# Kernel optimization log

Hardware: AMD Instinct MI355X
Metric: run time of the kernel (lower is better)

## Reference

```python
import jax, jax.numpy as jnp
import numpy as np
import math

D_MODEL = 1024
N_HEADS = 16
D_KV = 64
INNER = N_HEADS * D_KV
NUM_BUCKETS = 32
MAX_DISTANCE = 128


def _relative_position_bucket(relative_position, bidirectional=True,
                              num_buckets=NUM_BUCKETS, max_distance=MAX_DISTANCE):
    # faithful port of T5Attention._relative_position_bucket
    relative_buckets = jnp.zeros_like(relative_position)
    if bidirectional:
        num_buckets //= 2
        relative_buckets = relative_buckets + (relative_position > 0).astype(jnp.int32) * num_buckets
        relative_position = jnp.abs(relative_position)
    else:
        relative_position = -jnp.minimum(relative_position, jnp.zeros_like(relative_position))
    max_exact = num_buckets // 2
    is_small = relative_position < max_exact
    rp_large = max_exact + (
        jnp.log(relative_position.astype(jnp.float32) / max_exact)
        / math.log(max_distance / max_exact) * (num_buckets - max_exact)
    ).astype(jnp.int32)
    rp_large = jnp.minimum(rp_large, num_buckets - 1)
    return relative_buckets + jnp.where(is_small, relative_position, rp_large)


def compute_bias(rel_bias_table, q_len, k_len):
    # [q_len, k_len] relative positions -> bucket ids -> [1, H, q_len, k_len] bias
    context = jnp.arange(q_len, dtype=jnp.int32)[:, None]
    memory = jnp.arange(k_len, dtype=jnp.int32)[None, :]
    buckets = _relative_position_bucket(memory - context, bidirectional=True)
    values = rel_bias_table[buckets]            # [q, k, H]
    return jnp.transpose(values, (2, 0, 1))[None]  # [1, H, q, k]


def setup_inputs() -> dict:
    key = jax.random.key(0)
    ks = jax.random.split(key, 6)
    B, S = 2, 2048
    scale = 0.02
    return {
        "hidden_states": jax.random.normal(ks[0], (B, S, D_MODEL), jnp.float32),
        # weights stored as [in, out] (torch Linear applies x @ W.T with W [out,in])
        "w_q": jax.random.normal(ks[1], (D_MODEL, INNER), jnp.float32) * scale,
        "w_k": jax.random.normal(ks[2], (D_MODEL, INNER), jnp.float32) * scale,
        "w_v": jax.random.normal(ks[3], (D_MODEL, INNER), jnp.float32) * scale,
        "w_o": jax.random.normal(ks[4], (INNER, D_MODEL), jnp.float32) * scale,
        "rel_bias_table": jax.random.normal(ks[5], (NUM_BUCKETS, N_HEADS), jnp.float32) * scale,
    }


def reference(hidden_states, w_q, w_k, w_v, w_o, rel_bias_table):
    B, S, _ = hidden_states.shape

    def shape(x):  # [B, S, inner] -> [B, H, S, d_kv]
        return jnp.transpose(x.reshape(B, S, N_HEADS, D_KV), (0, 2, 1, 3))

    q = shape(hidden_states @ w_q)  # note: T5 applies no 1/sqrt(d) scaling
    k = shape(hidden_states @ w_k)
    v = shape(hidden_states @ w_v)

    scores = jnp.einsum("bhqd,bhkd->bhqk", q, k)
    position_bias = compute_bias(rel_bias_table, S, S)
    scores = scores + position_bias
    attn = jax.nn.softmax(scores.astype(jnp.float32), axis=-1).astype(scores.dtype)
    ctx = jnp.einsum("bhqk,bhkd->bhqd", attn, v)
    ctx = jnp.transpose(ctx, (0, 2, 1, 3)).reshape(B, S, INNER)
    return ctx @ w_o
```

## Files before the change

kernel.cpp:

```cpp
#include <hip/hip_runtime.h>
#include <math.h>

#define S_LEN 2048
#define DM 1024

typedef __attribute__((ext_vector_type(8))) __bf16 bf16x8;
typedef __attribute__((ext_vector_type(4))) float floatx4;

typedef __attribute__((address_space(1))) const unsigned int g_u32;
typedef __attribute__((address_space(3))) unsigned int l_u32;

__device__ __forceinline__ unsigned short f2bf(float f) {
  union { float f; unsigned int u; } v; v.f = f;
  return (unsigned short)((v.u + 0x7fffu + ((v.u >> 16) & 1u)) >> 16);
}
__device__ __forceinline__ float bf2f(unsigned short u) {
  union { unsigned int u; float f; } v; v.u = ((unsigned int)u) << 16;
  return v.f;
}
__device__ __forceinline__ bf16x8 ld_frag(const unsigned short* p) {
  union { uint4 u; bf16x8 v; } t;
  t.u = *(const uint4*)p;
  return t.v;
}

__global__ void detect_k(const unsigned short* __restrict__ x, int* __restrict__ flag) {
  __shared__ int cnt;
  if (threadIdx.x == 0) cnt = 0;
  __syncthreads();
  int local = 0;
  for (int i = threadIdx.x; i < 4096; i += 256) {
    unsigned short u = x[i];
    int e = (u >> 7) & 0xFF;
    if (e > 140) local++;
  }
  atomicAdd(&cnt, local);
  __syncthreads();
  if (threadIdx.x == 0) *flag = (cnt > 64) ? 1 : 0;
}

__global__ void conv_bias(const void* __restrict__ src, unsigned short* __restrict__ dst,
                          const void* __restrict__ table, float* __restrict__ outb,
                          const int* __restrict__ flag) {
  const int bid = blockIdx.x, tid = threadIdx.x;
  if (bid < 2048) {
    int i = bid * 256 + tid;
    if (*flag) {
      const float4* s = (const float4*)src;
      float4 a = s[2 * i], b = s[2 * i + 1];
      union { uint4 u4; unsigned short s[8]; } o;
      o.s[0] = f2bf(a.x); o.s[1] = f2bf(a.y); o.s[2] = f2bf(a.z); o.s[3] = f2bf(a.w);
      o.s[4] = f2bf(b.x); o.s[5] = f2bf(b.y); o.s[6] = f2bf(b.z); o.s[7] = f2bf(b.w);
      ((uint4*)dst)[i] = o.u4;
    } else {
      ((uint4*)dst)[i] = ((const uint4*)src)[i];
    }
  } else {
    int idx = (bid - 2048) * 256 + tid;
    if (idx >= 16 * 384) return;
    int h = idx / 384;
    int j = idx - h * 384;
    int delta = j - 192;
    int bucket = (delta > 0) ? 16 : 0;
    int ad = (delta < 0) ? -delta : delta;
    int smallv;
    if (ad < 8) smallv = ad;
    else {
      int l = (int)(log((double)ad * 0.125) * (8.0 / log(16.0)));
      smallv = 8 + l;
      if (smallv > 15) smallv = 15;
    }
    bucket += smallv;
    float v;
    if (*flag) v = ((const float*)table)[bucket * 16 + h];
    else       v = bf2f(((const unsigned short*)table)[bucket * 16 + h]);
    outb[idx] = v * 1.44269504f - 24.f;
  }
}

__global__ void transpose_w(const void* __restrict__ s0, const void* __restrict__ s1,
                            const void* __restrict__ s2, const void* __restrict__ s3,
                            unsigned short* __restrict__ Wcat, unsigned short* __restrict__ Wto,
                            const int* __restrict__ flag) {
  __shared__ float tile[32][33];
  const int z = blockIdx.z;
  const void* src = (z == 0) ? s0 : (z == 1) ? s1 : (z == 2) ? s2 : s3;
  unsigned short* dst = (z < 3) ? (Wcat + (size_t)z * 1048576) : Wto;
  const int isf = *flag;
  int x = blockIdx.x * 32 + threadIdx.x;
  int y0 = blockIdx.y * 32;
  for (int i = threadIdx.y; i < 32; i += 8) {
    float v;
    if (isf) v = ((const float*)src)[(size_t)(y0 + i) * DM + x];
    else     v = bf2f(((const unsigned short*)src)[(size_t)(y0 + i) * DM + x]);
    tile[i][threadIdx.x] = v;
  }
  __syncthreads();
  int xo = y0 + threadIdx.x;
  for (int i = threadIdx.y; i < 32; i += 8)
    dst[(size_t)(blockIdx.x * 32 + i) * DM + xo] = f2bf(tile[threadIdx.x][i]);
}

__global__ __launch_bounds__(256) void gemm_bt(
    const unsigned short* __restrict__ A, const unsigned short* __restrict__ Bt,
    void* __restrict__ C)
{
  __shared__ __align__(16) unsigned short smem[128 * 136];
  unsigned short* As = smem;
  unsigned short* Bs = smem + 8192;
  const int tid = threadIdx.x;
  const int lane = tid & 63, wave = tid >> 6;
  const int l16 = lane & 15, quad = lane >> 4;
  const int wm = (wave >> 1) << 6, wn = (wave & 1) << 6;
  const int m0 = blockIdx.y << 7, n0 = blockIdx.x << 7;
  const int lrow = lane >> 3, lcol = (lane & 7) << 3;

  floatx4 acc[4][4] = {};

  for (int k0 = 0; k0 < 1024; k0 += 64) {
    __syncthreads();
#pragma unroll
    for (int i = 0; i < 4; ++i) {
      int r0 = wave * 32 + i * 8;
      __builtin_amdgcn_global_load_lds(
          (g_u32*)(const void*)(A + (size_t)(m0 + r0 + lrow) * 1024 + k0 + lcol),
          (l_u32*)(void*)&As[r0 * 64], 16, 0, 0);
      __builtin_amdgcn_global_load_lds(
          (g_u32*)(const void*)(Bt + (size_t)(n0 + r0 + lrow) * 1024 + k0 + lcol),
          (l_u32*)(void*)&Bs[r0 * 64], 16, 0, 0);
    }
    __syncthreads();
#pragma unroll
    for (int ks = 0; ks < 2; ++ks) {
      bf16x8 a[4], b[4];
#pragma unroll
      for (int mi = 0; mi < 4; ++mi)
        a[mi] = *(const bf16x8*)&As[(wm + mi * 16 + l16) * 64 + ks * 32 + quad * 8];
#pragma unroll
      for (int ni = 0; ni < 4; ++ni)
        b[ni] = *(const bf16x8*)&Bs[(wn + ni * 16 + l16) * 64 + ks * 32 + quad * 8];
#pragma unroll
      for (int mi = 0; mi < 4; ++mi)
#pragma unroll
        for (int ni = 0; ni < 4; ++ni)
          acc[mi][ni] = __builtin_amdgcn_mfma_f32_16x16x32_bf16(a[mi], b[ni], acc[mi][ni], 0, 0, 0);
    }
  }

  unsigned short* Cs = (unsigned short*)C;
  const int mat = n0 >> 10;
  if (mat < 2) {
#pragma unroll
    for (int mi = 0; mi < 4; ++mi)
#pragma unroll
      for (int ni = 0; ni < 4; ++ni)
#pragma unroll
        for (int i = 0; i < 4; ++i) {
          int m = m0 + wm + mi * 16 + quad * 4 + i;
          int n = (n0 & 1023) + wn + ni * 16 + l16;
          int b = m >> 11, s = m & 2047, h = n >> 6, d = n & 63;
          Cs[(size_t)mat * 4194304 + (((size_t)(b * 16 + h)) * 2048 + s) * 64 + d] =
              f2bf(acc[mi][ni][i]);
        }
  } else {
    __syncthreads();
#pragma unroll
    for (int mi = 0; mi < 4; ++mi)
#pragma unroll
      for (int ni = 0; ni < 4; ++ni) {
        union { unsigned short s[4]; uint2 u; } w;
#pragma unroll
        for (int i = 0; i < 4; ++i) w.s[i] = f2bf(acc[mi][ni][i]);
        *(uint2*)&smem[(wn + ni * 16 + l16) * 136 + wm + mi * 16 + quad * 4] = w.u;
      }
    __syncthreads();
    const int bb = m0 >> 11, s0 = m0 & 2047, nb = n0 & 1023;
#pragma unroll
    for (int it = 0; it < 8; ++it) {
      int r = it * 16 + (tid >> 4);
      int c = (tid & 15) * 8;
      uint4 rv = *(const uint4*)&smem[r * 136 + c];
      *(uint4*)&Cs[(size_t)2 * 4194304 + (size_t)(bb * 1024 + nb + r) * 2048 + s0 + c] = rv;
    }
  }
}

__global__ __launch_bounds__(256) void gemm_out(
    const unsigned short* __restrict__ A, const unsigned short* __restrict__ Bt,
    void* __restrict__ C, const int* __restrict__ flag)
{
  __shared__ __align__(16) unsigned short As[128 * 64];
  __shared__ __align__(16) unsigned short Bs[64 * 64];
  const int tid = threadIdx.x;
  const int lane = tid & 63, wave = tid >> 6;
  const int l16 = lane & 15, quad = lane >> 4;
  const int wm = (wave >> 1) << 6, wn = (wave & 1) << 5;
  const int m0 = blockIdx.y << 7, n0 = blockIdx.x << 6;
  const int lrow = lane >> 3, lcol = (lane & 7) << 3;

  floatx4 acc[4][2] = {};

  for (int k0 = 0; k0 < 1024; k0 += 64) {
    __syncthreads();
#pragma unroll
    for (int i = 0; i < 4; ++i) {
      int r0 = wave * 32 + i * 8;
      __builtin_amdgcn_global_load_lds(
          (g_u32*)(const void*)(A + (size_t)(m0 + r0 + lrow) * 1024 + k0 + lcol),
          (l_u32*)(void*)&As[r0 * 64], 16, 0, 0);
    }
#pragma unroll
    for (int i = 0; i < 2; ++i) {
      int r0 = wave * 16 + i * 8;
      __builtin_amdgcn_global_load_lds(
          (g_u32*)(const void*)(Bt + (size_t)(n0 + r0 + lrow) * 1024 + k0 + lcol),
          (l_u32*)(void*)&Bs[r0 * 64], 16, 0, 0);
    }
    __syncthreads();
#pragma unroll
    for (int ks = 0; ks < 2; ++ks) {
      bf16x8 a[4], b[2];
#pragma unroll
      for (int mi = 0; mi < 4; ++mi)
        a[mi] = *(const bf16x8*)&As[(wm + mi * 16 + l16) * 64 + ks * 32 + quad * 8];
#pragma unroll
      for (int ni = 0; ni < 2; ++ni)
        b[ni] = *(const bf16x8*)&Bs[(wn + ni * 16 + l16) * 64 + ks * 32 + quad * 8];
#pragma unroll
      for (int mi = 0; mi < 4; ++mi)
#pragma unroll
        for (int ni = 0; ni < 2; ++ni)
          acc[mi][ni] = __builtin_amdgcn_mfma_f32_16x16x32_bf16(a[mi], b[ni], acc[mi][ni], 0, 0, 0);
    }
  }

  const int isf = *flag;
#pragma unroll
  for (int mi = 0; mi < 4; ++mi)
#pragma unroll
    for (int ni = 0; ni < 2; ++ni)
#pragma unroll
      for (int i = 0; i < 4; ++i) {
        int m = m0 + wm + mi * 16 + quad * 4 + i;
        int n = n0 + wn + ni * 16 + l16;
        size_t idx = (size_t)m * 1024 + n;
        float v = acc[mi][ni][i];
        if (isf) ((float*)C)[idx] = v;
        else     ((unsigned short*)C)[idx] = f2bf(v);
      }
}

#define STAGE_KV(kv0, buf)                                                    \
  {                                                                           \
    int rr = tid >> 3;                                                        \
    int sw = ((tid & 7) ^ (rr & 7)) << 3;                                     \
    __builtin_amdgcn_global_load_lds(                                         \
        (g_u32*)(const void*)(Kp + (size_t)((kv0) + rr) * 64 + sw),           \
        (l_u32*)(void*)&Ks[buf][wave * 512], 16, 0, 0);                       \
    __builtin_amdgcn_global_load_lds(                                         \
        (g_u32*)(const void*)(Vp + (size_t)rr * S_LEN + (kv0) + sw),          \
        (l_u32*)(void*)&Vs[buf][wave * 512], 16, 0, 0);                       \
  }

__global__ __launch_bounds__(512, 4) void attn_k(
    const unsigned short* __restrict__ Q, const unsigned short* __restrict__ K,
    const unsigned short* __restrict__ Vt, const float* __restrict__ bias,
    unsigned short* __restrict__ ctx)
{
  __shared__ __align__(16) unsigned short Ks[2][4096];
  __shared__ __align__(16) unsigned short Vs[2][4096];
  __shared__ __align__(16) unsigned short Ps[8][16][72];
  __shared__ float Bls[384];
  const int tid = threadIdx.x;
  const int lane = tid & 63, wave = tid >> 6;
  const int l16 = lane & 15, quad = lane >> 4;
  const int bh = blockIdx.y;
  const int b = bh >> 4, h = bh & 15;
  const int q0 = blockIdx.x << 7;
  const int wq = wave << 4;

  const unsigned short* Qp = Q + (size_t)bh * S_LEN * 64;
  const unsigned short* Kp = K + (size_t)bh * S_LEN * 64;
  const unsigned short* Vp = Vt + (size_t)bh * 64 * S_LEN;
  const float* biasg = bias + h * 384;

  STAGE_KV(0, 0);
  if (tid < 384) Bls[tid] = biasg[tid];

  bf16x8 qf[2];
#pragma unroll
  for (int ks = 0; ks < 2; ++ks)
    qf[ks] = ld_frag(Qp + (size_t)(q0 + wq + l16) * 64 + ks * 32 + quad * 8);

  float l_run[4] = {};
  floatx4 oacc[4] = {};

  const int qwb = q0 + wq;
  const int rbase = 192 + l16 - (quad << 2) - qwb;

  __syncthreads();
  const float Bneg = Bls[0], Bpos = Bls[383];

  for (int kv0 = 0; kv0 < S_LEN; kv0 += 64) {
    const int cur = (kv0 >> 6) & 1;
    if (kv0 + 64 < S_LEN) STAGE_KV(kv0 + 64, cur ^ 1);

    floatx4 sac[4] = {};
#pragma unroll
    for (int ks = 0; ks < 2; ++ks) {
      bf16x8 kf[4];
#pragma unroll
      for (int ni = 0; ni < 4; ++ni)
        kf[ni] = *(const bf16x8*)&Ks[cur][(ni * 16 + l16) * 64 +
                                          ((((ks << 2) + quad) ^ (l16 & 7)) << 3)];
#pragma unroll
      for (int ni = 0; ni < 4; ++ni)
        sac[ni] = __builtin_amdgcn_mfma_f32_16x16x32_bf16(qf[ks], kf[ni], sac[ni], 0, 0, 0);
    }

    {
      const int dmin = kv0 - (qwb + 15);
      const int dmax = kv0 + 63 - qwb;
      if (dmin >= 96 || dmax <= -96) {
        const float bc = (dmin >= 96) ? Bpos : Bneg;
#pragma unroll
        for (int i = 0; i < 4; ++i) {
          float sum = 0.f;
#pragma unroll
          for (int ni = 0; ni < 4; ++ni) {
            float e = __builtin_amdgcn_exp2f(fmaf(sac[ni][i], 1.44269504f, bc));
            sac[ni][i] = e; sum += e;
          }
          l_run[i] += sum;
        }
      } else {
#pragma unroll
        for (int i = 0; i < 4; ++i) {
          const int bbase = kv0 + rbase - i;
          float sum = 0.f;
#pragma unroll
          for (int ni = 0; ni < 4; ++ni) {
            float e = __builtin_amdgcn_exp2f(
                fmaf(sac[ni][i], 1.44269504f, Bls[bbase + ni * 16]));
            sac[ni][i] = e; sum += e;
          }
          l_run[i] += sum;
        }
      }
    }

#pragma unroll
    for (int ni = 0; ni < 4; ++ni)
#pragma unroll
      for (int i = 0; i < 4; ++i)
        Ps[wave][quad * 4 + i][ni * 16 + l16] = f2bf(sac[ni][i]);

#pragma unroll
    for (int ks2 = 0; ks2 < 2; ++ks2) {
      bf16x8 af, vf[4];
      af = *(const bf16x8*)&Ps[wave][l16][ks2 * 32 + quad * 8];
#pragma unroll
      for (int ni = 0; ni < 4; ++ni)
        vf[ni] = *(const bf16x8*)&Vs[cur][(ni * 16 + l16) * 64 +
                                          ((((ks2 << 2) + quad) ^ (l16 & 7)) << 3)];
#pragma unroll
      for (int ni = 0; ni < 4; ++ni)
        oacc[ni] = __builtin_amdgcn_mfma_f32_16x16x32_bf16(af, vf[ni], oacc[ni], 0, 0, 0);
    }

    __syncthreads();
  }

  float linv[4];
#pragma unroll
  for (int i = 0; i < 4; ++i) {
    float ls = l_run[i];
    ls += __shfl_xor(ls, 1);
    ls += __shfl_xor(ls, 2);
    ls += __shfl_xor(ls, 4);
    ls += __shfl_xor(ls, 8);
    linv[i] = 1.f / ls;
  }

#pragma unroll
  for (int ni = 0; ni < 4; ++ni)
#pragma unroll
    for (int i = 0; i < 4; ++i) {
      float v = oacc[ni][i] * linv[i];
      int srow = q0 + wq + quad * 4 + i;
      ctx[((size_t)(b * 2048 + srow)) * 1024 + h * 64 + ni * 16 + l16] = f2bf(v);
    }
}

extern "C" void kernel_launch(void* const* d_in, const int* in_sizes, int n_in,
                              void* d_out, int out_size, void* d_ws, size_t ws_size,
                              hipStream_t stream) {
  char* ws = (char*)d_ws;
  unsigned short* Xbf  = (unsigned short*)(ws);
  unsigned short* Wcat = (unsigned short*)(ws + 8388608);
  unsigned short* Wto  = (unsigned short*)(ws + 14680064);
  unsigned short* Qb   = (unsigned short*)(ws + 16777216);
  unsigned short* ctx  = (unsigned short*)(ws + 41943040);
  float*          bias = (float*)(ws + 50331648);
  int*            flag = (int*)(ws + 50593792);

  unsigned short* Kb  = Qb + 4194304;
  unsigned short* Vtb = Qb + 8388608;

  detect_k<<<1, 256, 0, stream>>>((const unsigned short*)d_in[0], flag);
  conv_bias<<<2072, 256, 0, stream>>>(d_in[0], Xbf, d_in[5], bias, flag);
  transpose_w<<<dim3(32, 32, 4), dim3(32, 8), 0, stream>>>(
      d_in[1], d_in[2], d_in[3], d_in[4], Wcat, Wto, flag);

  gemm_bt<<<dim3(24, 32), 256, 0, stream>>>(Xbf, Wcat, Qb);

  attn_k<<<dim3(16, 32), 512, 0, stream>>>(Qb, Kb, Vtb, bias, ctx);

  gemm_out<<<dim3(16, 32), 256, 0, stream>>>(ctx, Wto, d_out, flag);
}
```

Before: 222.4 us.

## Fuse prep kernels, compute softmax row sums via MFMA, use native bf16 convert

Merges the input conversion, bias table and weight transpose kernels into one prep launch, cutting launch overhead. Replaces the detect kernel with a host-side check on input size plus a memset when the size matches. In attention, the per-row exp sums are now taken by an extra MFMA against a ones vector instead of scalar adds and shuffles, which frees VALU work at the cost of one more MFMA per k-step. Float-to-bf16 conversion now uses the native cast.

```diff
diff --git a/kernel.cpp b/kernel.cpp
--- a/kernel.cpp
+++ b/kernel.cpp
@@ -11,8 +11,9 @@
 typedef __attribute__((address_space(3))) unsigned int l_u32;
 
 __device__ __forceinline__ unsigned short f2bf(float f) {
-  union { float f; unsigned int u; } v; v.f = f;
-  return (unsigned short)((v.u + 0x7fffu + ((v.u >> 16) & 1u)) >> 16);
+  union { __bf16 h; unsigned short u; } v;
+  v.h = (__bf16)f;
+  return v.u;
 }
 __device__ __forceinline__ float bf2f(unsigned short u) {
   union { unsigned int u; float f; } v; v.u = ((unsigned int)u) << 16;
@@ -39,23 +40,27 @@
   if (threadIdx.x == 0) *flag = (cnt > 64) ? 1 : 0;
 }
 
-__global__ void conv_bias(const void* __restrict__ src, unsigned short* __restrict__ dst,
-                          const void* __restrict__ table, float* __restrict__ outb,
-                          const int* __restrict__ flag) {
+__global__ void prep_k(const void* __restrict__ x, unsigned short* __restrict__ dst,
+                       const void* __restrict__ tbl, float* __restrict__ outb,
+                       const void* __restrict__ w0, const void* __restrict__ w1,
+                       const void* __restrict__ w2, const void* __restrict__ w3,
+                       unsigned short* __restrict__ Wcat, unsigned short* __restrict__ Wto,
+                       const int* __restrict__ flag) {
+  __shared__ float tile[32][33];
   const int bid = blockIdx.x, tid = threadIdx.x;
   if (bid < 2048) {
     int i = bid * 256 + tid;
     if (*flag) {
-      const float4* s = (const float4*)src;
+      const float4* s = (const float4*)x;
       float4 a = s[2 * i], b = s[2 * i + 1];
       union { uint4 u4; unsigned short s[8]; } o;
       o.s[0] = f2bf(a.x); o.s[1] = f2bf(a.y); o.s[2] = f2bf(a.z); o.s[3] = f2bf(a.w);
       o.s[4] = f2bf(b.x); o.s[5] = f2bf(b.y); o.s[6] = f2bf(b.z); o.s[7] = f2bf(b.w);
       ((uint4*)dst)[i] = o.u4;
     } else {
-      ((uint4*)dst)[i] = ((const uint4*)src)[i];
-    }
-  } else {
+      ((uint4*)dst)[i] = ((const uint4*)x)[i];
+    }
+  } else if (bid < 2072) {
     int idx = (bid - 2048) * 256 + tid;
     if (idx >= 16 * 384) return;
     int h = idx / 384;
@@ -72,33 +77,30 @@
     }
     bucket += smallv;
     float v;
-    if (*flag) v = ((const float*)table)[bucket * 16 + h];
-    else       v = bf2f(((const unsigned short*)table)[bucket * 16 + h]);
+    if (*flag) v = ((const float*)tbl)[bucket * 16 + h];
+    else       v = bf2f(((const unsigned short*)tbl)[bucket * 16 + h]);
     outb[idx] = v * 1.44269504f - 24.f;
-  }
-}
-
-__global__ void transpose_w(const void* __restrict__ s0, const void* __restrict__ s1,
-                            const void* __restrict__ s2, const void* __restrict__ s3,
-                            unsigned short* __restrict__ Wcat, unsigned short* __restrict__ Wto,
-                            const int* __restrict__ flag) {
-  __shared__ float tile[32][33];
-  const int z = blockIdx.z;
-  const void* src = (z == 0) ? s0 : (z == 1) ? s1 : (z == 2) ? s2 : s3;
-  unsigned short* dst = (z < 3) ? (Wcat + (size_t)z * 1048576) : Wto;
-  const int isf = *flag;
-  int x = blockIdx.x * 32 + threadIdx.x;
-  int y0 = blockIdx.y * 32;
-  for (int i = threadIdx.y; i < 32; i += 8) {
-    float v;
-    if (isf) v = ((const float*)src)[(size_t)(y0 + i) * DM + x];
-    else     v = bf2f(((const unsigned short*)src)[(size_t)(y0 + i) * DM + x]);
-    tile[i][threadIdx.x] = v;
-  }
-  __syncthreads();
-  int xo = y0 + threadIdx.x;
-  for (int i = threadIdx.y; i < 32; i += 8)
-    dst[(size_t)(blockIdx.x * 32 + i) * DM + xo] = f2bf(tile[threadIdx.x][i]);
+  } else {
+    const int t = bid - 2072;
+    const int z = t >> 10, rem = t & 1023;
+    const int bx = rem & 31, by = rem >> 5;
+    const int tx = tid & 31, ty = tid >> 5;
+    const void* src = (z == 0) ? w0 : (z == 1) ? w1 : (z == 2) ? w2 : w3;
+    unsigned short* dsty = (z < 3) ? (Wcat + (size_t)z * 1048576) : Wto;
+    const int isf = *flag;
+    int xc = bx * 32 + tx;
+    int y0 = by * 32;
+    for (int i = ty; i < 32; i += 8) {
+      float v;
+      if (isf) v = ((const float*)src)[(size_t)(y0 + i) * DM + xc];
+      else     v = bf2f(((const unsigned short*)src)[(size_t)(y0 + i) * DM + xc]);
+      tile[i][tx] = v;
+    }
+    __syncthreads();
+    int xo = y0 + tx;
+    for (int i = ty; i < 32; i += 8)
+      dsty[(size_t)(bx * 32 + i) * DM + xo] = f2bf(tile[tx][i]);
+  }
 }
 
 __global__ __launch_bounds__(256) void gemm_bt(
@@ -292,8 +294,16 @@
   for (int ks = 0; ks < 2; ++ks)
     qf[ks] = ld_frag(Qp + (size_t)(q0 + wq + l16) * 64 + ks * 32 + quad * 8);
 
-  float l_run[4] = {};
+  bf16x8 ones;
+  {
+    union { unsigned short s[8]; bf16x8 v; } o;
+#pragma unroll
+    for (int j = 0; j < 8; ++j) o.s[j] = 0x3F80;
+    ones = o.v;
+  }
+
   floatx4 oacc[4] = {};
+  floatx4 lacc = {};
 
   const int qwb = q0 + wq;
   const int rbase = 192 + l16 - (quad << 2) - qwb;
@@ -324,27 +334,18 @@
       if (dmin >= 96 || dmax <= -96) {
         const float bc = (dmin >= 96) ? Bpos : Bneg;
 #pragma unroll
-        for (int i = 0; i < 4; ++i) {
-          float sum = 0.f;
-#pragma unroll
-          for (int ni = 0; ni < 4; ++ni) {
-            float e = __builtin_amdgcn_exp2f(fmaf(sac[ni][i], 1.44269504f, bc));
-            sac[ni][i] = e; sum += e;
-          }
-          l_run[i] += sum;
-        }
+        for (int i = 0; i < 4; ++i)
+#pragma unroll
+          for (int ni = 0; ni < 4; ++ni)
+            sac[ni][i] = __builtin_amdgcn_exp2f(fmaf(sac[ni][i], 1.44269504f, bc));
       } else {
 #pragma unroll
         for (int i = 0; i < 4; ++i) {
           const int bbase = kv0 + rbase - i;
-          float sum = 0.f;
-#pragma unroll
-          for (int ni = 0; ni < 4; ++ni) {
-            float e = __builtin_amdgcn_exp2f(
+#pragma unroll
+          for (int ni = 0; ni < 4; ++ni)
+            sac[ni][i] = __builtin_amdgcn_exp2f(
                 fmaf(sac[ni][i], 1.44269504f, Bls[bbase + ni * 16]));
-            sac[ni][i] = e; sum += e;
-          }
-          l_run[i] += sum;
         }
       }
     }
@@ -366,6 +367,7 @@
 #pragma unroll
       for (int ni = 0; ni < 4; ++ni)
         oacc[ni] = __builtin_amdgcn_mfma_f32_16x16x32_bf16(af, vf[ni], oacc[ni], 0, 0, 0);
+      lacc = __builtin_amdgcn_mfma_f32_16x16x32_bf16(af, ones, lacc, 0, 0, 0);
     }
 
     __syncthreads();
@@ -373,14 +375,7 @@
 
   float linv[4];
 #pragma unroll
-  for (int i = 0; i < 4; ++i) {
-    float ls = l_run[i];
-    ls += __shfl_xor(ls, 1);
-    ls += __shfl_xor(ls, 2);
-    ls += __shfl_xor(ls, 4);
-    ls += __shfl_xor(ls, 8);
-    linv[i] = 1.f / ls;
-  }
+  for (int i = 0; i < 4; ++i) linv[i] = 1.f / lacc[i];
 
 #pragma unroll
   for (int ni = 0; ni < 4; ++ni)
@@ -407,10 +402,19 @@
   unsigned short* Kb  = Qb + 4194304;
   unsigned short* Vtb = Qb + 8388608;
 
-  detect_k<<<1, 256, 0, stream>>>((const unsigned short*)d_in[0], flag);
-  conv_bias<<<2072, 256, 0, stream>>>(d_in[0], Xbf, d_in[5], bias, flag);
-  transpose_w<<<dim3(32, 32, 4), dim3(32, 8), 0, stream>>>(
-      d_in[1], d_in[2], d_in[3], d_in[4], Wcat, Wto, flag);
+  int isf = -1;
+  if (in_sizes && n_in > 0) {
+    if (in_sizes[0] == 2 * 2048 * 1024 * 4) isf = 1;
+    else if (in_sizes[0] == 2 * 2048 * 1024 * 2) isf = 0;
+  }
+  if (isf < 0)
+    detect_k<<<1, 256, 0, stream>>>((const unsigned short*)d_in[0], flag);
+  else
+    hipMemsetAsync(flag, isf, sizeof(int), stream);
+
+  prep_k<<<6168, 256, 0, stream>>>(d_in[0], Xbf, d_in[5], bias,
+                                   d_in[1], d_in[2], d_in[3], d_in[4],
+                                   Wcat, Wto, flag);
 
   gemm_bt<<<dim3(24, 32), 256, 0, stream>>>(Xbf, Wcat, Qb);
 
```

Result: faster. 217.3 us (-2.3%).
